# Kernel optimization log

Measured on AMD Instinct MI355X. Metric: run time of the kernel, lower is better.

Reference implementation:

```python
import jax, jax.numpy as jnp
import numpy as np

N_NODES, N_EDGES = 16000, 256000
M_IN_S, M_IN_V = 16, 8   # input irreps: 16x0e + 8x1o (dim 40)
M_K_S, M_K_V = 8, 4      # key/query irreps: 8x0e + 4x1o
M_V_S, M_V_V = 16, 8     # value irreps: 16x0e + 8x1o
NUM_BASIS, R_CUT = 32, 2.5
SQ3 = 1.7320508075688772  # sqrt(3)


def _fc_net(r, W1, W2):
    # e3nn FullyConnectedNet([num_basis,16,numels], silu): weight-normalized linears
    h = jax.nn.silu(r @ (W1 / jnp.sqrt(jnp.float32(W1.shape[0]))))
    return h @ (W2 / jnp.sqrt(jnp.float32(W2.shape[0])))


def _edge_tp(xs, xv, y0, y1, w, m1s, m1v, mos, mov):
    # FullyConnectedTensorProduct(in1 = m1s x0e + m1v x1o, in2 = 1x0e + 1x1o,
    #   out = mos x0e + mov x1o), per-edge external weights w [E, numels].
    # Paths: 0e*0e->0e, 1o*1o->0e (dot/sqrt3), 0e*1o->1o, 1o*0e->1o.
    E = w.shape[0]
    n1, n2, n3 = m1s * mos, m1v * mos, m1s * mov
    w_ss = w[:, :n1].reshape(E, m1s, mos)
    w_vv = w[:, n1:n1 + n2].reshape(E, m1v, mos)
    w_sv = w[:, n1 + n2:n1 + n2 + n3].reshape(E, m1s, mov)
    w_vs = w[:, n1 + n2 + n3:].reshape(E, m1v, mov)
    inv = 1.0 / jnp.sqrt(jnp.float32(m1s + m1v))  # fan-in path normalization
    out_s = (jnp.einsum('ei,eio->eo', xs * y0[:, None], w_ss)
             + jnp.einsum('eic,ec,eio->eo', xv, y1, w_vv) / SQ3) * inv
    out_v = (jnp.einsum('ei,ec,eio->eoc', xs, y1, w_sv)
             + jnp.einsum('eic,eio->eoc', xv * y0[:, None, None], w_vs)) * inv
    return out_s, out_v


def _forward(pos, x, Wq_s, Wq_v, Wk1, Wk2, Wv1, Wv2, Ws_ss, Ws_vv, edge_src, edge_dst):
    xs, xv = x[:, :M_IN_S], x[:, M_IN_S:].reshape(-1, M_IN_V, 3)
    vec = pos[edge_dst] - pos[edge_src]                       # [E,3]
    d = jnp.linalg.norm(vec, axis=1)
    d_safe = jnp.maximum(d, 1e-6)
    # bessel radial basis with cutoff (soft_one_hot_linspace, basis='bessel') * sqrt(num_basis)
    n = jnp.arange(1, NUM_BASIS + 1, dtype=jnp.float32)
    rad = jnp.sqrt(2.0 / R_CUT) * jnp.sin(n[None] * jnp.pi * d_safe[:, None] / R_CUT) / d_safe[:, None]
    rad = jnp.where((d < R_CUT)[:, None], rad, 0.0) * jnp.sqrt(jnp.float32(NUM_BASIS))
    # spherical harmonics lmax=1, normalize=True, component normalization
    vh = vec / d_safe[:, None]
    y0, y1 = jnp.ones_like(d), SQ3 * vh
    # query projection (o3.Linear: per-irrep linear with 1/sqrt(fan_in))
    q_s = xs @ Wq_s / jnp.sqrt(jnp.float32(M_IN_S))           # [N, M_K_S]
    q_v = jnp.einsum('nic,io->noc', xv, Wq_v) / jnp.sqrt(jnp.float32(M_IN_V))
    # per-edge tensor-product weights from radial MLPs (shared_weights=False)
    wk = _fc_net(rad, Wk1, Wk2)                               # [E, 288]
    wv = _fc_net(rad, Wv1, Wv2)                               # [E, 576]
    xs_e, xv_e = xs[edge_src], xv[edge_src]
    k_s, k_v = _edge_tp(xs_e, xv_e, y0, y1, wk, M_IN_S, M_IN_V, M_K_S, M_K_V)
    v_s, v_v = _edge_tp(xs_e, xv_e, y0, y1, wv, M_IN_S, M_IN_V, M_V_S, M_V_V)
    # similarity tensor product (query x key -> 0e), shared internal weights
    fan = jnp.sqrt(jnp.float32(M_K_S * M_K_S + M_K_V * M_K_V))
    sim = (jnp.einsum('ei,ij,ej->e', q_s[edge_dst], Ws_ss, k_s)
           + jnp.einsum('eic,ij,ejc->e', q_v[edge_dst], Ws_vv, k_v) / SQ3) / fan
    # scatter softmax over incoming edges of each dst node
    attn = jnp.exp(sim)
    Z = jax.ops.segment_sum(attn, edge_dst, num_segments=N_NODES)
    a = attn / Z[edge_dst]
    # weighted scatter-sum aggregation
    out_s = jax.ops.segment_sum(a[:, None] * v_s, edge_dst, num_segments=N_NODES)
    out_v = jax.ops.segment_sum(a[:, None, None] * v_v, edge_dst, num_segments=N_NODES)
    return jnp.concatenate([out_s, out_v.reshape(N_NODES, -1)], axis=1)  # [N, 40]


def setup_inputs() -> dict:
    key = jax.random.key(0)
    ks = jax.random.split(key, 12)
    wk_numels = M_IN_S * M_K_S + M_IN_V * M_K_S + M_IN_S * M_K_V + M_IN_V * M_K_V  # 288
    wv_numels = M_IN_S * M_V_S + M_IN_V * M_V_S + M_IN_S * M_V_V + M_IN_V * M_V_V  # 576
    return {
        'pos': jax.random.uniform(ks[0], (N_NODES, 3), jnp.float32) * 3.0,
        'x': jax.random.normal(ks[1], (N_NODES, M_IN_S + 3 * M_IN_V), jnp.float32),
        'Wq_s': jax.random.normal(ks[2], (M_IN_S, M_K_S), jnp.float32),
        'Wq_v': jax.random.normal(ks[3], (M_IN_V, M_K_V), jnp.float32),
        'Wk1': jax.random.normal(ks[4], (NUM_BASIS, 16), jnp.float32),
        'Wk2': jax.random.normal(ks[5], (16, wk_numels), jnp.float32),
        'Wv1': jax.random.normal(ks[6], (NUM_BASIS, 16), jnp.float32),
        'Wv2': jax.random.normal(ks[7], (16, wv_numels), jnp.float32),
        'Ws_ss': jax.random.normal(ks[8], (M_K_S, M_K_S), jnp.float32) * 0.1,
        'Ws_vv': jax.random.normal(ks[9], (M_K_V, M_K_V), jnp.float32) * 0.1,
        'edge_src': jax.random.randint(ks[10], (N_EDGES,), 0, N_NODES),
        'edge_dst': jax.random.randint(ks[11], (N_EDGES,), 0, N_NODES),
    }


def reference(pos, x, Wq_s, Wq_v, Wk1, Wk2, Wv1, Wv2, Ws_ss, Ws_vv, edge_src, edge_dst):
    return _forward(pos, x, Wq_s, Wq_v, Wk1, Wk2, Wv1, Wv2, Ws_ss, Ws_vv, edge_src, edge_dst)
```

## Files before the change

### kernel.cpp

```cpp
#include <hip/hip_runtime.h>
#include <hip/hip_bf16.h>

#define N_NODES 16000
#define N_EDGES 256000

#define OFF_SD     0
#define OFF_SIMB   512000
#define OFF_CNT    768000
#define OFF_START  784000
#define OFF_CUR    800001
#define OFF_WB     816004
#define OFF_WBK    834436
#define OFF_QT     846724
#define OFF_Z      1006724

typedef _Float16 f16x2 __attribute__((ext_vector_type(2)));
typedef _Float16 f16x8v __attribute__((ext_vector_type(8)));
typedef float f32x4v __attribute__((ext_vector_type(4)));

__device__ __forceinline__ float fdot2f(f16x2 a, f16x2 b, float c) {
#if __has_builtin(__builtin_amdgcn_fdot2)
  return __builtin_amdgcn_fdot2(a, b, c, false);
#else
  return fmaf((float)a.x, (float)b.x, fmaf((float)a.y, (float)b.y, c));
#endif
}

__device__ __forceinline__ unsigned packh2(float a, float b) {
  union { unsigned u; f16x2 p; } v;
  v.p.x = (_Float16)a; v.p.y = (_Float16)b;
  return v.u;
}

__device__ __forceinline__ unsigned splat_half(unsigned x, unsigned sel) {
#if __has_builtin(__builtin_amdgcn_perm)
  return __builtin_amdgcn_perm(x, x, sel);
#else
  unsigned h = (sel == 0x03020302u) ? (x >> 16) : (x & 0xffffu);
  return h | (h << 16);
#endif
}

__device__ __forceinline__ void load_row40(const float* __restrict__ p, float* xr) {
  const float4* rp = reinterpret_cast<const float4*>(p);
#pragma unroll
  for (int q = 0; q < 10; ++q) {
    float4 f = rp[q];
    xr[4 * q + 0] = f.x; xr[4 * q + 1] = f.y; xr[4 * q + 2] = f.z; xr[4 * q + 3] = f.w;
  }
}

struct EdgeGeom { float vhx, vhy, vhz, y1x, y1y, y1z; };

__global__ void k_hist(const int* __restrict__ edst, int* __restrict__ cnt) {
  int e = blockIdx.x * 256 + threadIdx.x;
  atomicAdd(&cnt[edst[e]], 1);
}

__global__ void __launch_bounds__(1024) k_scan(const int* __restrict__ cnt,
                                               int* __restrict__ start, int* __restrict__ cur) {
  __shared__ int part[1024];
  int t = threadIdx.x;
  int base = t * 16;
  int local[16];
  int sum = 0;
#pragma unroll
  for (int i = 0; i < 16; ++i) {
    int idx = base + i;
    int c = (idx < N_NODES) ? cnt[idx] : 0;
    local[i] = sum; sum += c;
  }
  part[t] = sum;
  __syncthreads();
  for (int off = 1; off < 1024; off <<= 1) {
    int v = (t >= off) ? part[t - off] : 0;
    __syncthreads();
    part[t] += v;
    __syncthreads();
  }
  int prev = (t == 0) ? 0 : part[t - 1];
#pragma unroll
  for (int i = 0; i < 16; ++i) {
    int idx = base + i;
    if (idx < N_NODES) { int st = prev + local[i]; start[idx] = st; cur[idx] = st; }
  }
  if (t == 0) start[N_NODES] = N_EDGES;
}

__global__ void k_fill(const int* __restrict__ esrc, const int* __restrict__ edst,
                       int* __restrict__ cur, int2* __restrict__ sd) {
  int e = blockIdx.x * 256 + threadIdx.x;
  int d = edst[e];
  int slot = atomicAdd(&cur[d], 1);
  sd[slot] = make_int2(esrc[e], d);
}

__global__ void k_prepB(const float* __restrict__ Wv2, unsigned short* __restrict__ WB) {
  int idx = blockIdx.x * 256 + threadIdx.x;
  int j = idx & 7;
  int lane = (idx >> 3) & 63;
  int t3 = idx >> 9;
  int ct = t3 % 3, kk = t3 / 3;
  int q = lane >> 4, m = lane & 15;
  int row = 32 * kk + 8 * q + j;
  int col = 16 * ct + m;
  int t = row & 15;
  float v = 0.f;
  if (row < 256) {
    int i = row >> 4;
    if (col < 16)      v = Wv2[t * 576 + i * 16 + col];
    else if (col < 24) v = Wv2[t * 576 + 384 + i * 8 + (col - 16)];
  } else if (row < 384) {
    int i = (row - 256) >> 4;
    if (col < 16)      v = Wv2[t * 576 + 256 + i * 16 + col];
  } else {
    int part = (row - 384) >> 7;
    int i = ((row - 384) & 127) >> 4;
    int cb = 24 + 8 * part;
    if (col >= cb && col < cb + 8) v = Wv2[t * 576 + 512 + i * 8 + (col - cb)];
  }
  union { unsigned short u; _Float16 h; } cv;
  cv.h = (_Float16)(v * 0.051031036307982884f);
  WB[idx] = cv.u;
}

__global__ void k_prepBK(const float* __restrict__ Wk2, unsigned short* __restrict__ WBK) {
  int idx = blockIdx.x * 256 + threadIdx.x;
  int j = idx & 7;
  int lane = (idx >> 3) & 63;
  int t2 = idx >> 9;
  int ct = t2 & 1, kk = t2 >> 1;
  int q = lane >> 4, m = lane & 15;
  int row = 32 * kk + 8 * q + j;
  int col = 16 * ct + m;
  int t = row & 15;
  float v = 0.f;
  if (col < 24) {
    if (row < 256) {
      int i = row >> 4;
      if (col < 8)       v = Wk2[t * 288 + i * 8 + col];
      else if (col < 12) v = Wk2[t * 288 + 192 + i * 4 + (col - 8)];
    } else if (row < 384) {
      int i = (row - 256) >> 4;
      if (col < 8)       v = Wk2[t * 288 + 128 + i * 8 + col];
    } else {
      int c = (row - 384) >> 7;
      int i = ((row - 384) & 127) >> 4;
      int cb = 12 + 4 * c;
      if (col >= cb && col < cb + 4) v = Wk2[t * 288 + 256 + i * 4 + (col - cb)];
    }
  }
  union { unsigned short u; _Float16 h; } cv;
  cv.h = (_Float16)(v * 0.051031036307982884f);
  WBK[idx] = cv.u;
}

__global__ void __launch_bounds__(128) k_nodeq(
    const float* __restrict__ x,
    const float* __restrict__ Wq_s, const float* __restrict__ Wq_v,
    const float* __restrict__ Wss, const float* __restrict__ Wvv,
    unsigned short* __restrict__ QT) {
  __shared__ float Ls[240];
  for (int i = threadIdx.x; i < 240; i += 128) {
    float v;
    if (i < 128)      v = Wq_s[i] * 0.25f;
    else if (i < 160) v = Wq_v[i - 128] * 0.3535533905932738f;
    else if (i < 224) v = Wss[i - 160] * 0.11180339887498948f;
    else              v = Wvv[i - 224] * 0.06454972243679028f;
    Ls[i] = v;
  }
  __syncthreads();
  int n = blockIdx.x * 128 + threadIdx.x;
  float xd[40];
  load_row40(x + 40 * n, xd);
  float qd[8], qvd[12];
#pragma unroll
  for (int o = 0; o < 8; ++o) qd[o] = 0.f;
#pragma unroll
  for (int i = 0; i < 16; ++i)
#pragma unroll
    for (int o = 0; o < 8; ++o) qd[o] = fmaf(xd[i], Ls[8 * i + o], qd[o]);
#pragma unroll
  for (int k = 0; k < 12; ++k) qvd[k] = 0.f;
#pragma unroll
  for (int i = 0; i < 8; ++i)
#pragma unroll
    for (int o = 0; o < 4; ++o)
#pragma unroll
      for (int c = 0; c < 3; ++c)
        qvd[3 * o + c] = fmaf(xd[16 + 3 * i + c], Ls[128 + 4 * i + o], qvd[3 * o + c]);
  float qf[20];
#pragma unroll
  for (int j = 0; j < 8; ++j) {
    float t = 0.f;
#pragma unroll
    for (int i = 0; i < 8; ++i) t = fmaf(qd[i], Ls[160 + 8 * i + j], t);
    qf[j] = t;
  }
#pragma unroll
  for (int o = 0; o < 4; ++o)
#pragma unroll
    for (int c = 0; c < 3; ++c) {
      float t = 0.f;
#pragma unroll
      for (int i = 0; i < 4; ++i) t = fmaf(qvd[3 * i + c], Ls[224 + 4 * i + o], t);
      qf[8 + 3 * o + c] = t;
    }
  uint2* qp = (uint2*)(QT + 20 * n);
#pragma unroll
  for (int b = 0; b < 5; ++b) {
    uint2 st;
    st.x = packh2(qf[4 * b], qf[4 * b + 1]);
    st.y = packh2(qf[4 * b + 2], qf[4 * b + 3]);
    qp[b] = st;
  }
}

#define RSTR 36

__device__ __forceinline__ void build_coef(const float* xr, const float* Bv, float* coef) {
#pragma unroll
  for (int i = 0; i < 16; ++i) coef[i] = xr[i];
#pragma unroll
  for (int i = 0; i < 8; ++i) coef[16 + i] = Bv[i];
#pragma unroll
  for (int p = 0; p < 4; ++p)
#pragma unroll
    for (int c = 0; c < 3; ++c) {
      coef[24 + 8 * c + 2 * p]     = xr[16 + 6 * p + c];
      coef[24 + 8 * c + 2 * p + 1] = xr[16 + 6 * p + 3 + c];
    }
}

__global__ void __launch_bounds__(256) k_edge(
    const float* __restrict__ pos, const float* __restrict__ x,
    const float* __restrict__ Wk1, const float* __restrict__ Wv1,
    const unsigned short* __restrict__ WBK, const unsigned short* __restrict__ WB,
    const unsigned short* __restrict__ QT,
    const int2* __restrict__ sd, float* __restrict__ Z, float* __restrict__ out) {
  __shared__ __align__(16) unsigned LWK[256];
  __shared__ __align__(16) unsigned LWV[256];
  __shared__ __align__(16) unsigned SM[4][64 * RSTR];

  int wave = threadIdx.x >> 6, lane = threadIdx.x & 63;
  int q = lane >> 4, m = lane & 15;
  int q1 = q & 1;
  unsigned seld = (q >> 1) ? 0x03020302u : 0x01000100u;
  int slot = blockIdx.x * 256 + threadIdx.x;
  int2 e = sd[slot];
  int s = e.x, d = e.y;

  uint2 qraw[5];
  {
    const uint2* qp = (const uint2*)(QT + 20 * d);
#pragma unroll
    for (int b = 0; b < 5; ++b) qraw[b] = qp[b];
  }

  {
    int i = threadIdx.x;
    int bp = i >> 4, t = i & 15;
    LWK[i] = packh2(Wk1[(2 * bp) * 16 + t] * 0.17677669529663687f,
                    Wk1[(2 * bp + 1) * 16 + t] * 0.17677669529663687f);
    LWV[i] = packh2(Wv1[(2 * bp) * 16 + t] * 0.17677669529663687f,
                    Wv1[(2 * bp + 1) * 16 + t] * 0.17677669529663687f);
  }
  __syncthreads();

  bool same[6];
#pragma unroll
  for (int k = 0; k < 6; ++k) {
    int dd = __shfl_down(d, 1 << k, 64);
    same[k] = ((lane + (1 << k)) < 64) && (dd == d);
  }
  int dprev = __shfl_up(d, 1, 64);
  bool head = (lane == 0) || (dprev != d);

  union { uint4 u[2]; unsigned dd[8]; } hKp, hVp;
  EdgeGeom g;
  {
    float vx = pos[3 * d + 0] - pos[3 * s + 0];
    float vy = pos[3 * d + 1] - pos[3 * s + 1];
    float vz = pos[3 * d + 2] - pos[3 * s + 2];
    float dist = sqrtf(fmaf(vx, vx, fmaf(vy, vy, vz * vz)));
    float dsafe = fmaxf(dist, 1e-6f);
    float rinv = 1.0f / dsafe;
    g.vhx = vx * rinv; g.vhy = vy * rinv; g.vhz = vz * rinv;
    g.y1x = 1.7320508075688772f * g.vhx;
    g.y1y = 1.7320508075688772f * g.vhy;
    g.y1z = 1.7320508075688772f * g.vhz;
    float preK[16], preV[16];
#pragma unroll
    for (int t = 0; t < 16; ++t) { preK[t] = 0.f; preV[t] = 0.f; }
    float sx, cx;
    sincosf(1.2566370614359172f * dsafe, &sx, &cx);
    cx = fminf(1.f, fmaxf(-1.f, cx));
    float twoc = 2.f * cx;
    float sprev = 0.f, scur = sx;
    float rscale = (dist < 2.5f) ? (5.059644256269407f * rinv) : 0.f;
#pragma unroll
    for (int bp = 0; bp < 16; ++bp) {
      float r0 = rscale * scur;
      float sn = fmaf(twoc, scur, -sprev); sprev = scur; scur = sn;
      float r1 = rscale * scur;
      sn = fmaf(twoc, scur, -sprev); sprev = scur; scur = sn;
      union { unsigned u; f16x2 p; } rp; rp.p.x = (_Float16)r0; rp.p.y = (_Float16)r1;
      union { uint4 u[4]; f16x2 p[16]; } wk, wv;
      wk.u[0] = *(const uint4*)(LWK + bp * 16);
      wk.u[1] = *(const uint4*)(LWK + bp * 16 + 4);
      wk.u[2] = *(const uint4*)(LWK + bp * 16 + 8);
      wk.u[3] = *(const uint4*)(LWK + bp * 16 + 12);
      wv.u[0] = *(const uint4*)(LWV + bp * 16);
      wv.u[1] = *(const uint4*)(LWV + bp * 16 + 4);
      wv.u[2] = *(const uint4*)(LWV + bp * 16 + 8);
      wv.u[3] = *(const uint4*)(LWV + bp * 16 + 12);
#pragma unroll
      for (int t = 0; t < 16; ++t) {
        preK[t] = fdot2f(rp.p, wk.p[t], preK[t]);
        preV[t] = fdot2f(rp.p, wv.p[t], preV[t]);
      }
    }
#pragma unroll
    for (int tp = 0; tp < 8; ++tp) {
      float k0 = preK[2 * tp]     / (1.f + __expf(-preK[2 * tp]));
      float k1 = preK[2 * tp + 1] / (1.f + __expf(-preK[2 * tp + 1]));
      float v0 = preV[2 * tp]     / (1.f + __expf(-preV[2 * tp]));
      float v1 = preV[2 * tp + 1] / (1.f + __expf(-preV[2 * tp + 1]));
      hKp.dd[tp] = packh2(k0, k1);
      hVp.dd[tp] = packh2(v0, v1);
    }
  }

  float xr[40];
  load_row40(x + 40 * s, xr);
  float Bv[8];
#pragma unroll
  for (int i = 0; i < 8; ++i)
    Bv[i] = fmaf(xr[16 + 3 * i], g.vhx, fmaf(xr[17 + 3 * i], g.vhy, xr[18 + 3 * i] * g.vhz));
  float coef[48];
  build_coef(xr, Bv, coef);

  union { uint4 u[6]; unsigned dd[24]; } cfp;
#pragma unroll
  for (int bt = 0; bt < 6; ++bt) {
    cfp.dd[4 * bt + 0] = packh2(coef[8 * bt + 0], coef[8 * bt + 1]);
    cfp.dd[4 * bt + 1] = packh2(coef[8 * bt + 2], coef[8 * bt + 3]);
    cfp.dd[4 * bt + 2] = packh2(coef[8 * bt + 4], coef[8 * bt + 5]);
    cfp.dd[4 * bt + 3] = packh2(coef[8 * bt + 6], coef[8 * bt + 7]);
  }

  unsigned* row = &SM[wave][lane * RSTR];
  unsigned* wbase = &SM[wave][0];
  float* ctb = (float*)wbase;

  *(uint4*)(row)     = hKp.u[0];
  *(uint4*)(row + 4) = hKp.u[1];
#pragma unroll
  for (int bt = 0; bt < 6; ++bt) *(uint4*)(row + 8 + 4 * bt) = cfp.u[bt];

  union { uint4 u; f16x2 p[4]; } hs[4];
#pragma unroll
  for (int rt = 0; rt < 4; ++rt)
    hs[rt].u = *(const uint4*)(wbase + (16 * rt + m) * RSTR + 4 * q1);

  const uint4* WBKq = (const uint4*)WBK;
  f32x4v accK[4][2];
#pragma unroll
  for (int rt = 0; rt < 4; ++rt)
#pragma unroll
    for (int ct = 0; ct < 2; ++ct) { f32x4v z = {0.f, 0.f, 0.f, 0.f}; accK[rt][ct] = z; }

#pragma unroll
  for (int bt = 0; bt < 6; ++bt) {
    union { uint4 u; unsigned d[4]; } cb[4];
#pragma unroll
    for (int rt = 0; rt < 4; ++rt)
      cb[rt].u = *(const uint4*)(wbase + (16 * rt + m) * RSTR + 8 + 4 * bt);
#pragma unroll
    for (int t = 0; t < 4; ++t) {
      int kk = 4 * bt + t;
      union { uint4 u; f16x2 p[4]; f16x8v v; } av[4];
#pragma unroll
      for (int rt = 0; rt < 4; ++rt) {
        union { unsigned d; f16x2 p; } sp;
        sp.d = splat_half(cb[rt].d[t], seld);
#pragma unroll
        for (int w = 0; w < 4; ++w) av[rt].p[w] = hs[rt].p[w] * sp.p;
      }
#pragma unroll
      for (int ct = 0; ct < 2; ++ct) {
        union { uint4 u; f16x8v v; } bf;
        bf.u = WBKq[(kk * 2 + ct) * 64 + lane];
#pragma unroll
        for (int rt = 0; rt < 4; ++rt)
          accK[rt][ct] = __builtin_amdgcn_mfma_f32_16x16x32_f16(av[rt].v, bf.v, accK[rt][ct], 0, 0, 0);
      }
    }
  }

  float P[24];
#pragma unroll
  for (int rt = 0; rt < 4; ++rt)
#pragma unroll
    for (int r = 0; r < 4; ++r)
      ctb[m * 65 + 16 * rt + 4 * q + r] = accK[rt][0][r];
#pragma unroll
  for (int o = 0; o < 16; ++o) P[o] = ctb[o * 65 + lane];
#pragma unroll
  for (int rt = 0; rt < 4; ++rt)
#pragma unroll
    for (int r = 0; r < 4; ++r)
      ctb[m * 65 + 16 * rt + 4 * q + r] = accK[rt][1][r];
#pragma unroll
  for (int o = 0; o < 8; ++o) P[16 + o] = ctb[o * 65 + lane];

  float qf[20];
#pragma unroll
  for (int b = 0; b < 5; ++b) {
    union { unsigned d; f16x2 p; } a0, a1;
    a0.d = qraw[b].x; a1.d = qraw[b].y;
    qf[4 * b] = (float)a0.p.x; qf[4 * b + 1] = (float)a0.p.y;
    qf[4 * b + 2] = (float)a1.p.x; qf[4 * b + 3] = (float)a1.p.y;
  }

  float sim = 0.f;
#pragma unroll
  for (int j = 0; j < 8; ++j) sim = fmaf(qf[j], P[j], sim);
  float y1c[3] = {g.y1x, g.y1y, g.y1z};
#pragma unroll
  for (int o = 0; o < 4; ++o)
#pragma unroll
    for (int c = 0; c < 3; ++c)
      sim = fmaf(qf[8 + 3 * o + c], fmaf(y1c[c], P[8 + o], P[12 + 4 * c + o]), sim);
  float ev = __expf(sim);

  {
    float v = ev;
#pragma unroll
    for (int k = 0; k < 6; ++k) {
      float ov = __shfl_down(v, 1 << k, 64);
      v += same[k] ? ov : 0.f;
    }
    if (head) atomicAdd(&Z[d], v);
  }

  *(uint4*)(row)     = hVp.u[0];
  *(uint4*)(row + 4) = hVp.u[1];
#pragma unroll
  for (int bt = 0; bt < 6; ++bt) *(uint4*)(row + 8 + 4 * bt) = cfp.u[bt];

#pragma unroll
  for (int rt = 0; rt < 4; ++rt)
    hs[rt].u = *(const uint4*)(wbase + (16 * rt + m) * RSTR + 4 * q1);

  const uint4* WBq = (const uint4*)WB;
  f32x4v accV[4][3];
#pragma unroll
  for (int rt = 0; rt < 4; ++rt)
#pragma unroll
    for (int ct = 0; ct < 3; ++ct) { f32x4v z = {0.f, 0.f, 0.f, 0.f}; accV[rt][ct] = z; }

#pragma unroll
  for (int bt = 0; bt < 6; ++bt) {
    union { uint4 u; unsigned d[4]; } cb[4];
#pragma unroll
    for (int rt = 0; rt < 4; ++rt)
      cb[rt].u = *(const uint4*)(wbase + (16 * rt + m) * RSTR + 8 + 4 * bt);
#pragma unroll
    for (int t = 0; t < 4; ++t) {
      int kk = 4 * bt + t;
      union { uint4 u; f16x2 p[4]; f16x8v v; } av[4];
#pragma unroll
      for (int rt = 0; rt < 4; ++rt) {
        union { unsigned d; f16x2 p; } sp;
        sp.d = splat_half(cb[rt].d[t], seld);
#pragma unroll
        for (int w = 0; w < 4; ++w) av[rt].p[w] = hs[rt].p[w] * sp.p;
      }
#pragma unroll
      for (int ct = 0; ct < 3; ++ct) {
        union { uint4 u; f16x8v v; } bf;
        bf.u = WBq[(kk * 3 + ct) * 64 + lane];
#pragma unroll
        for (int rt = 0; rt < 4; ++rt)
          accV[rt][ct] = __builtin_amdgcn_mfma_f32_16x16x32_f16(av[rt].v, bf.v, accV[rt][ct], 0, 0, 0);
      }
    }
  }

  float* op = out + 40 * d;

  {
#pragma unroll
    for (int rt = 0; rt < 4; ++rt)
#pragma unroll
      for (int r = 0; r < 4; ++r)
        ctb[m * 65 + 16 * rt + 4 * q + r] = accV[rt][0][r];
    float P0[16];
#pragma unroll
    for (int o = 0; o < 16; ++o) P0[o] = ctb[o * 65 + lane];
#pragma unroll
    for (int o = 0; o < 16; ++o) {
      float v = ev * P0[o];
#pragma unroll
      for (int k = 0; k < 6; ++k) {
        float ov = __shfl_down(v, 1 << k, 64);
        v += same[k] ? ov : 0.f;
      }
      if (head) atomicAdd(op + o, v);
    }
  }
  float P1[16], P2[16];
#pragma unroll
  for (int rt = 0; rt < 4; ++rt)
#pragma unroll
    for (int r = 0; r < 4; ++r)
      ctb[m * 65 + 16 * rt + 4 * q + r] = accV[rt][1][r];
#pragma unroll
  for (int o = 0; o < 16; ++o) P1[o] = ctb[o * 65 + lane];
#pragma unroll
  for (int rt = 0; rt < 4; ++rt)
#pragma unroll
    for (int r = 0; r < 4; ++r)
      ctb[m * 65 + 16 * rt + 4 * q + r] = accV[rt][2][r];
#pragma unroll
  for (int o = 0; o < 16; ++o) P2[o] = ctb[o * 65 + lane];
#pragma unroll
  for (int o = 0; o < 8; ++o) {
    float s1v = P1[o];
    float vc[3];
    vc[0] = ev * fmaf(g.y1x, s1v, P1[8 + o]);
    vc[1] = ev * fmaf(g.y1y, s1v, P2[o]);
    vc[2] = ev * fmaf(g.y1z, s1v, P2[8 + o]);
#pragma unroll
    for (int c = 0; c < 3; ++c) {
      float v = vc[c];
#pragma unroll
      for (int k = 0; k < 6; ++k) {
        float ov = __shfl_down(v, 1 << k, 64);
        v += same[k] ? ov : 0.f;
      }
      if (head) atomicAdd(op + 16 + 3 * o + c, v);
    }
  }
}

__global__ void k_div(const float* __restrict__ Z, float* __restrict__ out) {
  int i = blockIdx.x * 256 + threadIdx.x;
  float z = Z[i / 40];
  if (z != 0.f) out[i] /= z;
}

extern "C" void kernel_launch(void* const* d_in, const int* in_sizes, int n_in,
                              void* d_out, int out_size, void* d_ws, size_t ws_size,
                              hipStream_t stream) {
  (void)in_sizes; (void)n_in; (void)out_size; (void)ws_size;
  const float* pos  = (const float*)d_in[0];
  const float* x    = (const float*)d_in[1];
  const float* Wq_s = (const float*)d_in[2];
  const float* Wq_v = (const float*)d_in[3];
  const float* Wk1  = (const float*)d_in[4];
  const float* Wk2  = (const float*)d_in[5];
  const float* Wv1  = (const float*)d_in[6];
  const float* Wv2  = (const float*)d_in[7];
  const float* Wss  = (const float*)d_in[8];
  const float* Wvv  = (const float*)d_in[9];
  const int* esrc = (const int*)d_in[10];
  const int* edst = (const int*)d_in[11];
  int*   wsi  = (int*)d_ws;
  float* wsf  = (float*)d_ws;
  float* out  = (float*)d_out;

  int2*  sd    = (int2*)(wsi + OFF_SD);
  int*   cnt   = wsi + OFF_CNT;
  int*   start = wsi + OFF_START;
  int*   cur   = wsi + OFF_CUR;
  unsigned short* WB  = (unsigned short*)(wsf + OFF_WB);
  unsigned short* WBK = (unsigned short*)(wsf + OFF_WBK);
  unsigned short* QT  = (unsigned short*)(wsf + OFF_QT);
  float* Z    = wsf + OFF_Z;

  hipMemsetAsync(cnt, 0, (size_t)N_NODES * sizeof(int), stream);
  hipMemsetAsync(Z, 0, (size_t)N_NODES * sizeof(float), stream);
  hipMemsetAsync(out, 0, (size_t)(N_NODES * 40) * sizeof(float), stream);
  k_prepB<<<144, 256, 0, stream>>>(Wv2, WB);
  k_prepBK<<<96, 256, 0, stream>>>(Wk2, WBK);
  k_nodeq<<<125, 128, 0, stream>>>(x, Wq_s, Wq_v, Wss, Wvv, QT);
  k_hist<<<1000, 256, 0, stream>>>(edst, cnt);
  k_scan<<<1, 1024, 0, stream>>>(cnt, start, cur);
  k_fill<<<1000, 256, 0, stream>>>(esrc, edst, cur, sd);
  k_edge<<<1000, 256, 0, stream>>>(pos, x, Wk1, Wv1, WBK, WB, QT, sd, Z, out);
  k_div<<<2500, 256, 0, stream>>>(Z, out);
}
```

Before: 246.5 us.

## Merge prep kernels and memsets into one launch, replace scan with atomic offsets

Folds the zeroing of Z/out, both weight-repacking kernels, the node query projection and the destination histogram into a single block-partitioned prep kernel, so two memsets and several launches go away. The single-block serial scan becomes a parallel kernel where each node claims its segment with an atomicAdd on a global counter. Segments are then no longer ordered by node id, but they stay contiguous per node. The edge kernel also stages the packed coefficients and value hidden features in a new shared-memory buffer instead of keeping them in registers. That buffer adds 32 KB of LDS per block and drops the launch bound, so occupancy may change.

```diff
diff --git a/kernel.cpp b/kernel.cpp
--- a/kernel.cpp
+++ b/kernel.cpp
@@ -13,6 +13,7 @@
 #define OFF_WBK    834436
 #define OFF_QT     846724
 #define OFF_Z      1006724
+#define OFF_GT     1022724
 
 typedef _Float16 f16x2 __attribute__((ext_vector_type(2)));
 typedef _Float16 f16x8v __attribute__((ext_vector_type(8)));
@@ -52,39 +53,10 @@
 
 struct EdgeGeom { float vhx, vhy, vhz, y1x, y1y, y1z; };
 
-__global__ void k_hist(const int* __restrict__ edst, int* __restrict__ cnt) {
-  int e = blockIdx.x * 256 + threadIdx.x;
-  atomicAdd(&cnt[edst[e]], 1);
-}
-
-__global__ void __launch_bounds__(1024) k_scan(const int* __restrict__ cnt,
-                                               int* __restrict__ start, int* __restrict__ cur) {
-  __shared__ int part[1024];
-  int t = threadIdx.x;
-  int base = t * 16;
-  int local[16];
-  int sum = 0;
-#pragma unroll
-  for (int i = 0; i < 16; ++i) {
-    int idx = base + i;
-    int c = (idx < N_NODES) ? cnt[idx] : 0;
-    local[i] = sum; sum += c;
-  }
-  part[t] = sum;
-  __syncthreads();
-  for (int off = 1; off < 1024; off <<= 1) {
-    int v = (t >= off) ? part[t - off] : 0;
-    __syncthreads();
-    part[t] += v;
-    __syncthreads();
-  }
-  int prev = (t == 0) ? 0 : part[t - 1];
-#pragma unroll
-  for (int i = 0; i < 16; ++i) {
-    int idx = base + i;
-    if (idx < N_NODES) { int st = prev + local[i]; start[idx] = st; cur[idx] = st; }
-  }
-  if (t == 0) start[N_NODES] = N_EDGES;
+__global__ void k_scan2(const int* __restrict__ cnt, int* __restrict__ cur,
+                        int* __restrict__ gtot) {
+  int n = blockIdx.x * 256 + threadIdx.x;
+  if (n < N_NODES) cur[n] = atomicAdd(gtot, cnt[n]);
 }
 
 __global__ void k_fill(const int* __restrict__ esrc, const int* __restrict__ edst,
@@ -95,125 +67,155 @@
   sd[slot] = make_int2(esrc[e], d);
 }
 
-__global__ void k_prepB(const float* __restrict__ Wv2, unsigned short* __restrict__ WB) {
-  int idx = blockIdx.x * 256 + threadIdx.x;
-  int j = idx & 7;
-  int lane = (idx >> 3) & 63;
-  int t3 = idx >> 9;
-  int ct = t3 % 3, kk = t3 / 3;
-  int q = lane >> 4, m = lane & 15;
-  int row = 32 * kk + 8 * q + j;
-  int col = 16 * ct + m;
-  int t = row & 15;
-  float v = 0.f;
-  if (row < 256) {
-    int i = row >> 4;
-    if (col < 16)      v = Wv2[t * 576 + i * 16 + col];
-    else if (col < 24) v = Wv2[t * 576 + 384 + i * 8 + (col - 16)];
-  } else if (row < 384) {
-    int i = (row - 256) >> 4;
-    if (col < 16)      v = Wv2[t * 576 + 256 + i * 16 + col];
-  } else {
-    int part = (row - 384) >> 7;
-    int i = ((row - 384) & 127) >> 4;
-    int cb = 24 + 8 * part;
-    if (col >= cb && col < cb + 8) v = Wv2[t * 576 + 512 + i * 8 + (col - cb)];
-  }
-  union { unsigned short u; _Float16 h; } cv;
-  cv.h = (_Float16)(v * 0.051031036307982884f);
-  WB[idx] = cv.u;
-}
-
-__global__ void k_prepBK(const float* __restrict__ Wk2, unsigned short* __restrict__ WBK) {
-  int idx = blockIdx.x * 256 + threadIdx.x;
-  int j = idx & 7;
-  int lane = (idx >> 3) & 63;
-  int t2 = idx >> 9;
-  int ct = t2 & 1, kk = t2 >> 1;
-  int q = lane >> 4, m = lane & 15;
-  int row = 32 * kk + 8 * q + j;
-  int col = 16 * ct + m;
-  int t = row & 15;
-  float v = 0.f;
-  if (col < 24) {
-    if (row < 256) {
-      int i = row >> 4;
-      if (col < 8)       v = Wk2[t * 288 + i * 8 + col];
-      else if (col < 12) v = Wk2[t * 288 + 192 + i * 4 + (col - 8)];
-    } else if (row < 384) {
-      int i = (row - 256) >> 4;
-      if (col < 8)       v = Wk2[t * 288 + 128 + i * 8 + col];
-    } else {
-      int c = (row - 384) >> 7;
-      int i = ((row - 384) & 127) >> 4;
-      int cb = 12 + 4 * c;
-      if (col >= cb && col < cb + 4) v = Wk2[t * 288 + 256 + i * 4 + (col - cb)];
-    }
-  }
-  union { unsigned short u; _Float16 h; } cv;
-  cv.h = (_Float16)(v * 0.051031036307982884f);
-  WBK[idx] = cv.u;
-}
-
-__global__ void __launch_bounds__(128) k_nodeq(
+#define PREP_ZERO_B   2563
+#define PREP_PB_B     144
+#define PREP_PBK_B    96
+#define PREP_NQ_B     63
+#define PREP_HIST_B   1000
+#define PREP_TOTAL_B  (PREP_ZERO_B + PREP_PB_B + PREP_PBK_B + PREP_NQ_B + PREP_HIST_B)
+
+__global__ void __launch_bounds__(256) k_prep(
     const float* __restrict__ x,
     const float* __restrict__ Wq_s, const float* __restrict__ Wq_v,
     const float* __restrict__ Wss, const float* __restrict__ Wvv,
-    unsigned short* __restrict__ QT) {
-  __shared__ float Ls[240];
-  for (int i = threadIdx.x; i < 240; i += 128) {
-    float v;
-    if (i < 128)      v = Wq_s[i] * 0.25f;
-    else if (i < 160) v = Wq_v[i - 128] * 0.3535533905932738f;
-    else if (i < 224) v = Wss[i - 160] * 0.11180339887498948f;
-    else              v = Wvv[i - 224] * 0.06454972243679028f;
-    Ls[i] = v;
-  }
-  __syncthreads();
-  int n = blockIdx.x * 128 + threadIdx.x;
-  float xd[40];
-  load_row40(x + 40 * n, xd);
-  float qd[8], qvd[12];
-#pragma unroll
-  for (int o = 0; o < 8; ++o) qd[o] = 0.f;
-#pragma unroll
-  for (int i = 0; i < 16; ++i)
-#pragma unroll
-    for (int o = 0; o < 8; ++o) qd[o] = fmaf(xd[i], Ls[8 * i + o], qd[o]);
-#pragma unroll
-  for (int k = 0; k < 12; ++k) qvd[k] = 0.f;
-#pragma unroll
-  for (int i = 0; i < 8; ++i)
+    const float* __restrict__ Wk2, const float* __restrict__ Wv2,
+    const int* __restrict__ edst,
+    int* __restrict__ cnt, float* __restrict__ Z, float* __restrict__ out,
+    unsigned short* __restrict__ WB, unsigned short* __restrict__ WBK,
+    unsigned short* __restrict__ QT, int* __restrict__ gtot) {
+  int b = blockIdx.x;
+  if (b < PREP_ZERO_B) {
+    int i = b * 256 + threadIdx.x;
+    if (i < 16000)        Z[i] = 0.f;
+    else if (i < 656000)  out[i - 16000] = 0.f;
+    else if (i == 656000) *gtot = 0;
+    return;
+  }
+  b -= PREP_ZERO_B;
+  if (b < PREP_PB_B) {
+    int idx = b * 256 + threadIdx.x;
+    int j = idx & 7;
+    int lane = (idx >> 3) & 63;
+    int t3 = idx >> 9;
+    int ct = t3 % 3, kk = t3 / 3;
+    int q = lane >> 4, m = lane & 15;
+    int row = 32 * kk + 8 * q + j;
+    int col = 16 * ct + m;
+    int t = row & 15;
+    float v = 0.f;
+    if (row < 256) {
+      int i = row >> 4;
+      if (col < 16)      v = Wv2[t * 576 + i * 16 + col];
+      else if (col < 24) v = Wv2[t * 576 + 384 + i * 8 + (col - 16)];
+    } else if (row < 384) {
+      int i = (row - 256) >> 4;
+      if (col < 16)      v = Wv2[t * 576 + 256 + i * 16 + col];
+    } else {
+      int part = (row - 384) >> 7;
+      int i = ((row - 384) & 127) >> 4;
+      int cb = 24 + 8 * part;
+      if (col >= cb && col < cb + 8) v = Wv2[t * 576 + 512 + i * 8 + (col - cb)];
+    }
+    union { unsigned short u; _Float16 h; } cv;
+    cv.h = (_Float16)(v * 0.051031036307982884f);
+    WB[idx] = cv.u;
+    return;
+  }
+  b -= PREP_PB_B;
+  if (b < PREP_PBK_B) {
+    int idx = b * 256 + threadIdx.x;
+    int j = idx & 7;
+    int lane = (idx >> 3) & 63;
+    int t2 = idx >> 9;
+    int ct = t2 & 1, kk = t2 >> 1;
+    int q = lane >> 4, m = lane & 15;
+    int row = 32 * kk + 8 * q + j;
+    int col = 16 * ct + m;
+    int t = row & 15;
+    float v = 0.f;
+    if (col < 24) {
+      if (row < 256) {
+        int i = row >> 4;
+        if (col < 8)       v = Wk2[t * 288 + i * 8 + col];
+        else if (col < 12) v = Wk2[t * 288 + 192 + i * 4 + (col - 8)];
+      } else if (row < 384) {
+        int i = (row - 256) >> 4;
+        if (col < 8)       v = Wk2[t * 288 + 128 + i * 8 + col];
+      } else {
+        int c = (row - 384) >> 7;
+        int i = ((row - 384) & 127) >> 4;
+        int cb = 12 + 4 * c;
+        if (col >= cb && col < cb + 4) v = Wk2[t * 288 + 256 + i * 4 + (col - cb)];
+      }
+    }
+    union { unsigned short u; _Float16 h; } cv;
+    cv.h = (_Float16)(v * 0.051031036307982884f);
+    WBK[idx] = cv.u;
+    return;
+  }
+  b -= PREP_PBK_B;
+  if (b < PREP_NQ_B) {
+    __shared__ float Ls[240];
+    if (threadIdx.x < 240) {
+      int i = threadIdx.x;
+      float v;
+      if (i < 128)      v = Wq_s[i] * 0.25f;
+      else if (i < 160) v = Wq_v[i - 128] * 0.3535533905932738f;
+      else if (i < 224) v = Wss[i - 160] * 0.11180339887498948f;
+      else              v = Wvv[i - 224] * 0.06454972243679028f;
+      Ls[i] = v;
+    }
+    __syncthreads();
+    int n = b * 256 + threadIdx.x;
+    if (n >= N_NODES) return;
+    float xd[40];
+    load_row40(x + 40 * n, xd);
+    float qd[8], qvd[12];
+#pragma unroll
+    for (int o = 0; o < 8; ++o) qd[o] = 0.f;
+#pragma unroll
+    for (int i = 0; i < 16; ++i)
+#pragma unroll
+      for (int o = 0; o < 8; ++o) qd[o] = fmaf(xd[i], Ls[8 * i + o], qd[o]);
+#pragma unroll
+    for (int k = 0; k < 12; ++k) qvd[k] = 0.f;
+#pragma unroll
+    for (int i = 0; i < 8; ++i)
+#pragma unroll
+      for (int o = 0; o < 4; ++o)
+#pragma unroll
+        for (int c = 0; c < 3; ++c)
+          qvd[3 * o + c] = fmaf(xd[16 + 3 * i + c], Ls[128 + 4 * i + o], qvd[3 * o + c]);
+    float qf[20];
+#pragma unroll
+    for (int j = 0; j < 8; ++j) {
+      float t = 0.f;
+#pragma unroll
+      for (int i = 0; i < 8; ++i) t = fmaf(qd[i], Ls[160 + 8 * i + j], t);
+      qf[j] = t;
+    }
 #pragma unroll
     for (int o = 0; o < 4; ++o)
 #pragma unroll
-      for (int c = 0; c < 3; ++c)
-        qvd[3 * o + c] = fmaf(xd[16 + 3 * i + c], Ls[128 + 4 * i + o], qvd[3 * o + c]);
-  float qf[20];
-#pragma unroll
-  for (int j = 0; j < 8; ++j) {
-    float t = 0.f;
-#pragma unroll
-    for (int i = 0; i < 8; ++i) t = fmaf(qd[i], Ls[160 + 8 * i + j], t);
-    qf[j] = t;
-  }
-#pragma unroll
-  for (int o = 0; o < 4; ++o)
-#pragma unroll
-    for (int c = 0; c < 3; ++c) {
-      float t = 0.f;
-#pragma unroll
-      for (int i = 0; i < 4; ++i) t = fmaf(qvd[3 * i + c], Ls[224 + 4 * i + o], t);
-      qf[8 + 3 * o + c] = t;
-    }
-  uint2* qp = (uint2*)(QT + 20 * n);
-#pragma unroll
-  for (int b = 0; b < 5; ++b) {
-    uint2 st;
-    st.x = packh2(qf[4 * b], qf[4 * b + 1]);
-    st.y = packh2(qf[4 * b + 2], qf[4 * b + 3]);
-    qp[b] = st;
-  }
+      for (int c = 0; c < 3; ++c) {
+        float t = 0.f;
+#pragma unroll
+        for (int i = 0; i < 4; ++i) t = fmaf(qvd[3 * i + c], Ls[224 + 4 * i + o], t);
+        qf[8 + 3 * o + c] = t;
+      }
+    uint2* qp = (uint2*)(QT + 20 * n);
+#pragma unroll
+    for (int bq = 0; bq < 5; ++bq) {
+      uint2 st;
+      st.x = packh2(qf[4 * bq], qf[4 * bq + 1]);
+      st.y = packh2(qf[4 * bq + 2], qf[4 * bq + 3]);
+      qp[bq] = st;
+    }
+    return;
+  }
+  b -= PREP_NQ_B;
+  int e = b * 256 + threadIdx.x;
+  atomicAdd(&cnt[edst[e]], 1);
 }
 
 #define RSTR 36
@@ -232,7 +234,7 @@
     }
 }
 
-__global__ void __launch_bounds__(256) k_edge(
+__global__ void k_edge(
     const float* __restrict__ pos, const float* __restrict__ x,
     const float* __restrict__ Wk1, const float* __restrict__ Wv1,
     const unsigned short* __restrict__ WBK, const unsigned short* __restrict__ WB,
@@ -241,6 +243,7 @@
   __shared__ __align__(16) unsigned LWK[256];
   __shared__ __align__(16) unsigned LWV[256];
   __shared__ __align__(16) unsigned SM[4][64 * RSTR];
+  __shared__ __align__(16) unsigned PR[4][64 * 32];
 
   int wave = threadIdx.x >> 6, lane = threadIdx.x & 63;
   int q = lane >> 4, m = lane & 15;
@@ -340,23 +343,25 @@
   float coef[48];
   build_coef(xr, Bv, coef);
 
-  union { uint4 u[6]; unsigned dd[24]; } cfp;
-#pragma unroll
-  for (int bt = 0; bt < 6; ++bt) {
-    cfp.dd[4 * bt + 0] = packh2(coef[8 * bt + 0], coef[8 * bt + 1]);
-    cfp.dd[4 * bt + 1] = packh2(coef[8 * bt + 2], coef[8 * bt + 3]);
-    cfp.dd[4 * bt + 2] = packh2(coef[8 * bt + 4], coef[8 * bt + 5]);
-    cfp.dd[4 * bt + 3] = packh2(coef[8 * bt + 6], coef[8 * bt + 7]);
-  }
-
   unsigned* row = &SM[wave][lane * RSTR];
+  unsigned* prow = &PR[wave][lane * 32];
   unsigned* wbase = &SM[wave][0];
   float* ctb = (float*)wbase;
 
-  *(uint4*)(row)     = hKp.u[0];
-  *(uint4*)(row + 4) = hKp.u[1];
-#pragma unroll
-  for (int bt = 0; bt < 6; ++bt) *(uint4*)(row + 8 + 4 * bt) = cfp.u[bt];
+#pragma unroll
+  for (int bt = 0; bt < 6; ++bt) {
+    uint4 w;
+    w.x = packh2(coef[8 * bt + 0], coef[8 * bt + 1]);
+    w.y = packh2(coef[8 * bt + 2], coef[8 * bt + 3]);
+    w.z = packh2(coef[8 * bt + 4], coef[8 * bt + 5]);
+    w.w = packh2(coef[8 * bt + 6], coef[8 * bt + 7]);
+    *(uint4*)(row + 8 + 4 * bt) = w;
+    *(uint4*)(prow + 4 * bt) = w;
+  }
+  *(uint4*)(row)      = hKp.u[0];
+  *(uint4*)(row + 4)  = hKp.u[1];
+  *(uint4*)(prow + 24) = hVp.u[0];
+  *(uint4*)(prow + 28) = hVp.u[1];
 
   union { uint4 u; f16x2 p[4]; } hs[4];
 #pragma unroll
@@ -444,10 +449,17 @@
     if (head) atomicAdd(&Z[d], v);
   }
 
-  *(uint4*)(row)     = hVp.u[0];
-  *(uint4*)(row + 4) = hVp.u[1];
-#pragma unroll
-  for (int bt = 0; bt < 6; ++bt) *(uint4*)(row + 8 + 4 * bt) = cfp.u[bt];
+#pragma unroll
+  for (int bt = 0; bt < 6; ++bt) {
+    uint4 w = *(const uint4*)(prow + 4 * bt);
+    *(uint4*)(row + 8 + 4 * bt) = w;
+  }
+  {
+    uint4 h0 = *(const uint4*)(prow + 24);
+    uint4 h1 = *(const uint4*)(prow + 28);
+    *(uint4*)(row)     = h0;
+    *(uint4*)(row + 4) = h1;
+  }
 
 #pragma unroll
   for (int rt = 0; rt < 4; ++rt)
@@ -573,21 +585,17 @@
 
   int2*  sd    = (int2*)(wsi + OFF_SD);
   int*   cnt   = wsi + OFF_CNT;
-  int*   start = wsi + OFF_START;
   int*   cur   = wsi + OFF_CUR;
   unsigned short* WB  = (unsigned short*)(wsf + OFF_WB);
   unsigned short* WBK = (unsigned short*)(wsf + OFF_WBK);
   unsigned short* QT  = (unsigned short*)(wsf + OFF_QT);
   float* Z    = wsf + OFF_Z;
+  int*   gtot = wsi + OFF_GT;
 
   hipMemsetAsync(cnt, 0, (size_t)N_NODES * sizeof(int), stream);
-  hipMemsetAsync(Z, 0, (size_t)N_NODES * sizeof(float), stream);
-  hipMemsetAsync(out, 0, (size_t)(N_NODES * 40) * sizeof(float), stream);
-  k_prepB<<<144, 256, 0, stream>>>(Wv2, WB);
-  k_prepBK<<<96, 256, 0, stream>>>(Wk2, WBK);
-  k_nodeq<<<125, 128, 0, stream>>>(x, Wq_s, Wq_v, Wss, Wvv, QT);
-  k_hist<<<1000, 256, 0, stream>>>(edst, cnt);
-  k_scan<<<1, 1024, 0, stream>>>(cnt, start, cur);
+  k_prep<<<PREP_TOTAL_B, 256, 0, stream>>>(x, Wq_s, Wq_v, Wss, Wvv, Wk2, Wv2, edst,
+                                           cnt, Z, out, WB, WBK, QT, gtot);
+  k_scan2<<<63, 256, 0, stream>>>(cnt, cur, gtot);
   k_fill<<<1000, 256, 0, stream>>>(esrc, edst, cur, sd);
   k_edge<<<1000, 256, 0, stream>>>(pos, x, Wk1, Wv1, WBK, WB, QT, sd, Z, out);
   k_div<<<2500, 256, 0, stream>>>(Z, out);
```

Measured after the change: 246.6 us. No clear change (+0.0%).
